# Performance work log

Hardware: AMD Instinct MI355X
Metric: run time of the kernel (lower is better)

The kernel has to match this reference:

```python
import jax, jax.numpy as jnp
import numpy as np

N_NODES = 50000
BN_EPS = 1e-5


def setup_inputs() -> dict:
    key = jax.random.key(0)
    ks = jax.random.split(key, 16)
    N, IN, H, OUT, E = N_NODES, 512, 128, 64, 800000
    s = lambda fi, fo: 1.0 / np.sqrt(fi)
    inp = {
        'x': jax.random.normal(ks[0], (N, IN), dtype=jnp.float32),
        'edge_index': jax.random.randint(ks[1], (2, E), 0, N, dtype=jnp.int32),
        # mlpA: Linear(N -> H)
        'WA': jax.random.uniform(ks[2], (H, N), jnp.float32, -s(N, H), s(N, H)),
        'bA': jax.random.uniform(ks[3], (H,), jnp.float32, -s(N, H), s(N, H)),
        # mlpX: Linear(IN -> H)
        'WX': jax.random.uniform(ks[4], (H, IN), jnp.float32, -s(IN, H), s(IN, H)),
        'bX': jax.random.uniform(ks[5], (H,), jnp.float32, -s(IN, H), s(IN, H)),
        # W: Linear(2H -> H)
        'W': jax.random.uniform(ks[6], (H, 2 * H), jnp.float32, -s(2 * H, H), s(2 * H, H)),
        'bW': jax.random.uniform(ks[7], (H,), jnp.float32, -s(2 * H, H), s(2 * H, H)),
        # mlp_final layer 1: Linear(H -> H) + BN
        'Wf1': jax.random.uniform(ks[8], (H, H), jnp.float32, -s(H, H), s(H, H)),
        'bf1': jax.random.uniform(ks[9], (H,), jnp.float32, -s(H, H), s(H, H)),
        'gamma': jnp.ones((H,), jnp.float32),
        'beta': jnp.zeros((H,), jnp.float32),
        # mlp_final layer 2: Linear(H -> OUT)
        'Wf2': jax.random.uniform(ks[10], (OUT, H), jnp.float32, -s(H, OUT), s(H, OUT)),
        'bf2': jax.random.uniform(ks[11], (OUT,), jnp.float32, -s(H, OUT), s(H, OUT)),
    }
    return inp


def _batchnorm(x, gamma, beta):
    # training-mode BN over the node/batch axis (biased variance, as in torch)
    mean = jnp.mean(x, axis=0)
    var = jnp.var(x, axis=0)
    return (x - mean) * jax.lax.rsqrt(var + BN_EPS) * gamma + beta


def reference(x, edge_index, WA, bA, WX, bX, W, bW, Wf1, bf1, gamma, beta, Wf2, bf2):
    row, col = edge_index[0], edge_index[1]
    row = row - row.min()
    # xA = A @ WA.T + bA  where A[i,j]=1 per (row,col) edge (duplicates sum).
    # Equivalent SpMM: gather columns of WA at `col`, segment-sum into `row`.
    xA = jax.ops.segment_sum(WA.T[col], row, num_segments=N_NODES) + bA  # [N, H]
    xX = x @ WX.T + bX  # [N, H]
    h = jnp.concatenate([xA, xX], axis=-1) @ W.T + bW  # [N, H]
    h = jax.nn.relu(h + xA + xX)
    # mlp_final (num_layers=2): Linear -> ReLU -> BN -> (dropout off) -> Linear
    h = jax.nn.relu(h @ Wf1.T + bf1)
    h = _batchnorm(h, gamma, beta)
    out = h @ Wf2.T + bf2  # [N, OUT]
    return out
```

## Files before the change

kernel.cpp:

```cpp
#include <hip/hip_runtime.h>

typedef __bf16 bf16_t;
typedef __bf16 bf16x8 __attribute__((ext_vector_type(8)));
typedef __bf16 bf16x2 __attribute__((ext_vector_type(2)));
typedef float f32x4 __attribute__((ext_vector_type(4)));

#define IN_DIM 512
#define H_DIM 128
#define OUT_DIM 64
#define BN_EPS 1e-5f
#define SCAN_BLK 2048

#define MFMA(a, b, c) __builtin_amdgcn_mfma_f32_16x16x32_bf16(a, b, c, 0, 0, 0)

__device__ __forceinline__ int detect_bf(const void* gamma) {
    return (*(const unsigned*)gamma == 0x3F803F80u) ? 1 : 0;
}

__device__ __forceinline__ float ld_adapt(const void* p, size_t i, int isbf) {
    return isbf ? (float)((const bf16_t*)p)[i] : ((const float*)p)[i];
}

__device__ __forceinline__ void split8(const float* p, bf16x8& hi, bf16x8& lo) {
    f32x4 v0 = *(const f32x4*)p;
    f32x4 v1 = *(const f32x4*)(p + 4);
#pragma unroll
    for (int i = 0; i < 8; ++i) {
        float f = (i < 4) ? v0[i] : v1[i - 4];
        bf16_t h = (bf16_t)f;
        hi[i] = h;
        lo[i] = (bf16_t)(f - (float)h);
    }
}

__device__ __forceinline__ void split8v(const f32x4& v0, const f32x4& v1, bf16x8& hi, bf16x8& lo) {
#pragma unroll
    for (int i = 0; i < 8; ++i) {
        float f = (i < 4) ? v0[i] : v1[i - 4];
        bf16_t h = (bf16_t)f;
        hi[i] = h;
        lo[i] = (bf16_t)(f - (float)h);
    }
}

__global__ __launch_bounds__(256) void k_transpose(const void* __restrict__ WA,
                                                   void* __restrict__ WAT, int N,
                                                   const void* __restrict__ gamma) {
    __shared__ float t[64][130];
    int isbf = detect_bf(gamma);
    int n0 = blockIdx.x * 64;
    int tid = threadIdx.x;
#pragma unroll
    for (int i = 0; i < 32; ++i) {
        int lin = i * 256 + tid;
        int h = lin >> 6, nl = lin & 63;
        int n = n0 + nl;
        t[nl][h] = (n < N) ? ld_adapt(WA, (size_t)h * N + n, isbf) : 0.f;
    }
    __syncthreads();
#pragma unroll
    for (int i = 0; i < 32; ++i) {
        int lin = i * 256 + tid;
        int nl = lin >> 7, h = lin & 127;
        int n = n0 + nl;
        if (n < N) {
            float v = t[nl][h];
            if (isbf)
                ((bf16_t*)WAT)[(size_t)n * H_DIM + h] = (bf16_t)v;
            else
                ((float*)WAT)[(size_t)n * H_DIM + h] = v;
        }
    }
}

__global__ __launch_bounds__(256) void k_prep(const int* __restrict__ rows, int E,
                                              int* __restrict__ bmin, int* __restrict__ cnt) {
    __shared__ int sm[4];
    int i = blockIdx.x * 256 + threadIdx.x;
    int m = 0x7fffffff;
    if (i < E) {
        int r = rows[i];
        m = r;
        atomicAdd(&cnt[r], 1);
    }
    for (int off = 32; off; off >>= 1) m = min(m, __shfl_xor(m, off, 64));
    if ((threadIdx.x & 63) == 0) sm[threadIdx.x >> 6] = m;
    __syncthreads();
    if (threadIdx.x == 0)
        bmin[blockIdx.x] = min(min(sm[0], sm[1]), min(sm[2], sm[3]));
}

__global__ __launch_bounds__(256) void k_scan1(const int* __restrict__ cnt,
                                               int* __restrict__ offs,
                                               int* __restrict__ bsum, int N) {
    __shared__ int ts[256];
    int base = blockIdx.x * SCAN_BLK;
    int t = threadIdx.x;
    int v[8], s = 0;
#pragma unroll
    for (int i = 0; i < 8; ++i) {
        int idx = base + t * 8 + i;
        v[i] = (idx < N) ? cnt[idx] : 0;
        s += v[i];
    }
    ts[t] = s;
    __syncthreads();
    for (int off = 1; off < 256; off <<= 1) {
        int x = (t >= off) ? ts[t - off] : 0;
        __syncthreads();
        ts[t] += x;
        __syncthreads();
    }
    int run = ts[t] - s;
#pragma unroll
    for (int i = 0; i < 8; ++i) {
        int idx = base + t * 8 + i;
        if (idx < N) offs[idx] = run;
        run += v[i];
    }
    if (t == 255) bsum[blockIdx.x] = ts[255];
}

__global__ __launch_bounds__(256) void k_scan2(int* __restrict__ bsum, int* __restrict__ offs,
                                               int NB, int N, const int* __restrict__ bmin,
                                               int nbmin, int* __restrict__ minbuf) {
    __shared__ int sm[256];
    int t = threadIdx.x;
    int m = 0x7fffffff;
    for (int i = t; i < nbmin; i += 256) m = min(m, bmin[i]);
    sm[t] = m;
    __syncthreads();
    for (int off = 128; off; off >>= 1) {
        if (t < off) sm[t] = min(sm[t], sm[t + off]);
        __syncthreads();
    }
    if (t == 0) {
        *minbuf = sm[0];
        int run = 0;
        for (int b = 0; b < NB; ++b) {
            int v = bsum[b];
            bsum[b] = run;
            run += v;
        }
        offs[N] = run;
    }
}

__global__ __launch_bounds__(256) void k_scan3(int* __restrict__ offs, const int* __restrict__ bsum,
                                               int* __restrict__ cursor, int N) {
    int i = blockIdx.x * 256 + threadIdx.x;
    if (i >= N) return;
    int v = offs[i] + bsum[i / SCAN_BLK];
    offs[i] = v;
    cursor[i] = v;
}

__global__ __launch_bounds__(256) void k_build(const int* __restrict__ rows,
                                               const int* __restrict__ cols, int E,
                                               int* __restrict__ cursor,
                                               int* __restrict__ scol) {
    int i = blockIdx.x * 256 + threadIdx.x;
    if (i >= E) return;
    int r = rows[i];
    int pos = atomicAdd(&cursor[r], 1);
    scol[pos] = cols[i];
}

__global__ __launch_bounds__(256) void k_gather(const int* __restrict__ offs,
                                                const int* __restrict__ scol,
                                                const void* __restrict__ WAT,
                                                const void* __restrict__ bA,
                                                const int* __restrict__ minbuf,
                                                float* __restrict__ xA, int N,
                                                const void* __restrict__ gamma) {
    int isbf = detect_bf(gamma);
    int wave = threadIdx.x >> 6, lane = threadIdx.x & 63;
    int r = blockIdx.x * 4 + wave;
    if (r >= N) return;
    int b = r + *minbuf;
    int s = 0, e = 0;
    if (b < N) {
        s = offs[b];
        e = offs[b + 1];
    }
    float2 a0 = {0.f, 0.f}, a1 = {0.f, 0.f}, a2 = {0.f, 0.f}, a3 = {0.f, 0.f};
    int i = s;
    if (isbf) {
        const bf16_t* Wb = (const bf16_t*)WAT;
        for (; i + 7 < e; i += 8) {
            bf16x2 w[8];
#pragma unroll
            for (int j = 0; j < 8; ++j) {
                int c = scol[i + j];
                w[j] = *(const bf16x2*)(Wb + (size_t)c * H_DIM + lane * 2);
            }
            a0.x += (float)w[0][0] + (float)w[4][0]; a0.y += (float)w[0][1] + (float)w[4][1];
            a1.x += (float)w[1][0] + (float)w[5][0]; a1.y += (float)w[1][1] + (float)w[5][1];
            a2.x += (float)w[2][0] + (float)w[6][0]; a2.y += (float)w[2][1] + (float)w[6][1];
            a3.x += (float)w[3][0] + (float)w[7][0]; a3.y += (float)w[3][1] + (float)w[7][1];
        }
        for (; i < e; ++i) {
            int c = scol[i];
            bf16x2 w = *(const bf16x2*)(Wb + (size_t)c * H_DIM + lane * 2);
            a0.x += (float)w[0]; a0.y += (float)w[1];
        }
    } else {
        const float* Wf = (const float*)WAT;
        for (; i + 7 < e; i += 8) {
            float2 w[8];
#pragma unroll
            for (int j = 0; j < 8; ++j) {
                int c = scol[i + j];
                w[j] = *(const float2*)(Wf + (size_t)c * H_DIM + lane * 2);
            }
            a0.x += w[0].x + w[4].x; a0.y += w[0].y + w[4].y;
            a1.x += w[1].x + w[5].x; a1.y += w[1].y + w[5].y;
            a2.x += w[2].x + w[6].x; a2.y += w[2].y + w[6].y;
            a3.x += w[3].x + w[7].x; a3.y += w[3].y + w[7].y;
        }
        for (; i < e; ++i) {
            int c = scol[i];
            float2 w = *(const float2*)(Wf + (size_t)c * H_DIM + lane * 2);
            a0.x += w.x; a0.y += w.y;
        }
    }
    float bx = ld_adapt(bA, lane * 2, isbf);
    float by = ld_adapt(bA, lane * 2 + 1, isbf);
    float2 out = {a0.x + a1.x + a2.x + a3.x + bx, a0.y + a1.y + a2.y + a3.y + by};
    *(float2*)(xA + (size_t)r * H_DIM + lane * 2) = out;
}

__device__ __forceinline__ void pack_frag(const void* __restrict__ W, bf16_t* __restrict__ hi,
                                          bf16_t* __restrict__ lo, int K, int NC,
                                          int addres, int isbf, int f, int lane) {
    int ks = f / (NC >> 4), nt = f % (NC >> 4);
    int n = nt * 16 + (lane & 15);
    int k0 = ks * 32 + (lane >> 4) * 8;
    bf16_t* dh = hi + (size_t)f * 512 + lane * 8;
    bf16_t* dl = lo + (size_t)f * 512 + lane * 8;
#pragma unroll
    for (int j = 0; j < 8; ++j) {
        int kk = k0 + j;
        float v = ld_adapt(W, (size_t)n * K + kk, isbf);
        if (addres && (kk == n || kk == n + H_DIM)) v += 1.f;
        bf16_t h = (bf16_t)v;
        dh[j] = h;
        dl[j] = (bf16_t)(v - (float)h);
    }
}

__global__ __launch_bounds__(256) void k_pack3(const void* WX, bf16_t* WXh, bf16_t* WXl,
                                               const void* W, bf16_t* Wh, bf16_t* Wl,
                                               const void* Wf1, bf16_t* Wf1h, bf16_t* Wf1l,
                                               const void* __restrict__ gamma) {
    int g = blockIdx.x * 256 + threadIdx.x;
    int f = g >> 6, lane = g & 63;
    int isbf = detect_bf(gamma);
    if (f < 128)
        pack_frag(WX, WXh, WXl, IN_DIM, H_DIM, 0, isbf, f, lane);
    else if (f < 192)
        pack_frag(W, Wh, Wl, 2 * H_DIM, H_DIM, 1, isbf, f - 128, lane);
    else if (f < 224)
        pack_frag(Wf1, Wf1h, Wf1l, H_DIM, H_DIM, 0, isbf, f - 192, lane);
}

template <int ISBF>
__device__ __forceinline__ void fuseA_body(
    const void* __restrict__ x, const float* __restrict__ xAf,
    const bf16_t* __restrict__ WXh, const bf16_t* __restrict__ WXl,
    const bf16_t* __restrict__ Wh, const bf16_t* __restrict__ Wl,
    const bf16_t* __restrict__ Wf1h, const bf16_t* __restrict__ Wf1l,
    const void* __restrict__ bX, const void* __restrict__ bWv, const void* __restrict__ bf1,
    float* __restrict__ h2, double* __restrict__ sums, double* __restrict__ sumsq,
    float* ax, float* ls_sum, float* ls_sq, int M) {
    int tid = threadIdx.x;
    int wave = tid >> 6, lane = tid & 63, l16 = lane & 15, quad = lane >> 4;
    int band = wave & 1, half = wave >> 1;
    int ntb = half * 4;
    int mbase = blockIdx.x * 32 + band * 16;
    int r0 = min(mbase + l16, M - 1);

    if (tid < H_DIM) {
        ls_sum[tid] = 0.f;
        ls_sq[tid] = 0.f;
    }

    f32x4 acc[4];
    bf16x8 pb[2][4];

    auto loadB4 = [&](const bf16_t* __restrict__ H, int fb, bf16x8 dst[4]) {
        const bf16_t* hp = H + (size_t)fb * 512 + lane * 8;
#pragma unroll
        for (int nt = 0; nt < 4; ++nt) dst[nt] = *(const bf16x8*)(hp + nt * 512);
    };

#pragma unroll
    for (int nt = 0; nt < 4; ++nt) acc[nt] = f32x4{0.f, 0.f, 0.f, 0.f};
    if (ISBF) {
        const bf16_t* xb = (const bf16_t*)x + (size_t)r0 * IN_DIM + quad * 8;
        bf16x8 a[16];
#pragma unroll
        for (int ks = 0; ks < 16; ++ks) a[ks] = *(const bf16x8*)(xb + ks * 32);
        loadB4(WXh, ntb, pb[0]);
#pragma unroll
        for (int ks = 0; ks < 16; ++ks) {
            int cur = ks & 1;
            if (ks < 15) loadB4(WXh, (ks + 1) * 8 + ntb, pb[cur ^ 1]);
#pragma unroll
            for (int nt = 0; nt < 4; ++nt) acc[nt] = MFMA(a[ks], pb[cur][nt], acc[nt]);
        }
    } else {
        const float* xf = (const float*)x + (size_t)r0 * IN_DIM + quad * 8;
        bf16x8 bl4[4];
        for (int ks = 0; ks < 16; ++ks) {
            bf16x8 ah, al;
            split8(xf + ks * 32, ah, al);
            loadB4(WXh, ks * 8 + ntb, pb[0]);
            loadB4(WXl, ks * 8 + ntb, bl4);
#pragma unroll
            for (int nt = 0; nt < 4; ++nt) {
                acc[nt] = MFMA(ah, pb[0][nt], acc[nt]);
                acc[nt] = MFMA(ah, bl4[nt], acc[nt]);
                acc[nt] = MFMA(al, pb[0][nt], acc[nt]);
            }
        }
    }
#pragma unroll
    for (int nt = 0; nt < 4; ++nt) {
        int col = (ntb + nt) * 16 + l16;
        float b = ld_adapt(bX, col, ISBF);
#pragma unroll
        for (int r = 0; r < 4; ++r) {
            int lr = band * 16 + quad * 4 + r;
            ax[lr * 132 + col] = acc[nt][r] + b;
        }
    }
    __syncthreads();

#pragma unroll
    for (int nt = 0; nt < 4; ++nt) acc[nt] = f32x4{0.f, 0.f, 0.f, 0.f};
    {
        size_t aoff = (size_t)r0 * H_DIM + quad * 8;
        const float* axp = ax + (band * 16 + l16) * 132 + quad * 8;
        f32x4 pa[8];
#pragma unroll
        for (int i = 0; i < 8; ++i) pa[i] = *(const f32x4*)(xAf + aoff + (i >> 1) * 32 + (i & 1) * 4);
        bf16x8 bl4[4];
        loadB4(Wh, ntb, pb[0]);
#pragma unroll
        for (int ks = 0; ks < 8; ++ks) {
            int cur = ks & 1;
            if (ks < 7) loadB4(Wh, (ks + 1) * 8 + ntb, pb[cur ^ 1]);
            bf16x8 ah, al;
            if (ks < 4)
                split8v(pa[2 * ks], pa[2 * ks + 1], ah, al);
            else
                split8(axp + (ks - 4) * 32, ah, al);
            if (!ISBF) loadB4(Wl, ks * 8 + ntb, bl4);
#pragma unroll
            for (int nt = 0; nt < 4; ++nt) {
                acc[nt] = MFMA(ah, pb[cur][nt], acc[nt]);
                acc[nt] = MFMA(al, pb[cur][nt], acc[nt]);
                if (!ISBF) acc[nt] = MFMA(ah, bl4[nt], acc[nt]);
            }
        }
    }
    __syncthreads();
#pragma unroll
    for (int nt = 0; nt < 4; ++nt) {
        int col = (ntb + nt) * 16 + l16;
        float b = ld_adapt(bWv, col, ISBF);
#pragma unroll
        for (int r = 0; r < 4; ++r) {
            int lr = band * 16 + quad * 4 + r;
            ax[lr * 132 + col] = fmaxf(acc[nt][r] + b, 0.f);
        }
    }
    __syncthreads();

#pragma unroll
    for (int nt = 0; nt < 4; ++nt) acc[nt] = f32x4{0.f, 0.f, 0.f, 0.f};
    {
        const float* axp = ax + (band * 16 + l16) * 132 + quad * 8;
        bf16x8 bl4[4];
        loadB4(Wf1h, ntb, pb[0]);
#pragma unroll
        for (int ks = 0; ks < 4; ++ks) {
            int cur = ks & 1;
            if (ks < 3) loadB4(Wf1h, (ks + 1) * 8 + ntb, pb[cur ^ 1]);
            bf16x8 ah, al;
            split8(axp + ks * 32, ah, al);
            if (!ISBF) loadB4(Wf1l, ks * 8 + ntb, bl4);
#pragma unroll
            for (int nt = 0; nt < 4; ++nt) {
                acc[nt] = MFMA(ah, pb[cur][nt], acc[nt]);
                acc[nt] = MFMA(al, pb[cur][nt], acc[nt]);
                if (!ISBF) acc[nt] = MFMA(ah, bl4[nt], acc[nt]);
            }
        }
    }
#pragma unroll
    for (int nt = 0; nt < 4; ++nt) {
        int col = (ntb + nt) * 16 + l16;
        float b = ld_adapt(bf1, col, ISBF);
        float s = 0.f, s2 = 0.f;
#pragma unroll
        for (int r = 0; r < 4; ++r) {
            int row = mbase + quad * 4 + r;
            if (row < M) {
                float v = fmaxf(acc[nt][r] + b, 0.f);
                h2[(size_t)row * H_DIM + col] = v;
                s += v;
                s2 += v * v;
            }
        }
        s += __shfl_xor(s, 16, 64);
        s += __shfl_xor(s, 32, 64);
        s2 += __shfl_xor(s2, 16, 64);
        s2 += __shfl_xor(s2, 32, 64);
        if (quad == 0) {
            atomicAdd(&ls_sum[col], s);
            atomicAdd(&ls_sq[col], s2);
        }
    }
    __syncthreads();
    if (tid < H_DIM) {
        atomicAdd(&sums[tid], (double)ls_sum[tid]);
        atomicAdd(&sumsq[tid], (double)ls_sq[tid]);
    }
}

__global__ __launch_bounds__(256, 4) void k_fuseA(
    const void* __restrict__ x, const float* __restrict__ xAf,
    const bf16_t* __restrict__ WXh, const bf16_t* __restrict__ WXl,
    const bf16_t* __restrict__ Wh, const bf16_t* __restrict__ Wl,
    const bf16_t* __restrict__ Wf1h, const bf16_t* __restrict__ Wf1l,
    const void* __restrict__ bX, const void* __restrict__ bWv, const void* __restrict__ bf1,
    float* __restrict__ h2, double* __restrict__ sums, double* __restrict__ sumsq,
    const void* __restrict__ gamma, int M) {
    __shared__ float ax[32 * 132];
    __shared__ float ls_sum[H_DIM], ls_sq[H_DIM];
    if (detect_bf(gamma))
        fuseA_body<1>(x, xAf, WXh, WXl, Wh, Wl, Wf1h, Wf1l, bX, bWv, bf1, h2, sums, sumsq,
                      ax, ls_sum, ls_sq, M);
    else
        fuseA_body<0>(x, xAf, WXh, WXl, Wh, Wl, Wf1h, Wf1l, bX, bWv, bf1, h2, sums, sumsq,
                      ax, ls_sum, ls_sq, M);
}

__global__ __launch_bounds__(256) void k_fuseB(
    const float* __restrict__ h2, const void* __restrict__ Wf2,
    const void* __restrict__ gamma, const void* __restrict__ beta, const void* __restrict__ bf2,
    const double* __restrict__ sums, const double* __restrict__ sumsq,
    void* __restrict__ outv, int M) {
    __shared__ bf16_t wh[16 * 512];
    __shared__ bf16_t wl[16 * 512];
    __shared__ float aw[H_DIM], cw[H_DIM], b2[OUT_DIM];
    int t = threadIdx.x;
    int isbf = detect_bf(gamma);

    if (t < H_DIM) {
        double mean = sums[t] / (double)M;
        double var = sumsq[t] / (double)M - mean * mean;
        if (var < 0) var = 0;
        float a = ld_adapt(gamma, t, isbf) * rsqrtf((float)var + BN_EPS);
        aw[t] = a;
        cw[t] = ld_adapt(beta, t, isbf) - (float)mean * a;
    }
    __syncthreads();
    if (t < OUT_DIM) {
        float acc = ld_adapt(bf2, t, isbf);
        for (int j = 0; j < H_DIM; ++j) acc += ld_adapt(Wf2, (size_t)t * H_DIM + j, isbf) * cw[j];
        b2[t] = acc;
    }
    for (int u = t; u < 1024; u += 256) {
        int f = u >> 6, ln = u & 63;
        int ks = f >> 2, nt = f & 3;
        int n = nt * 16 + (ln & 15);
        int k0 = ks * 32 + (ln >> 4) * 8;
#pragma unroll
        for (int j = 0; j < 8; ++j) {
            float v = ld_adapt(Wf2, (size_t)n * H_DIM + k0 + j, isbf) * aw[k0 + j];
            bf16_t h = (bf16_t)v;
            wh[f * 512 + ln * 8 + j] = h;
            wl[f * 512 + ln * 8 + j] = (bf16_t)(v - (float)h);
        }
    }
    __syncthreads();

    int wave = t >> 6, lane = t & 63, l16 = lane & 15, quad = lane >> 4;
    int mbase = blockIdx.x * 64 + wave * 16;
    int r0 = min(mbase + l16, M - 1);
    f32x4 ph[8];
#pragma unroll
    for (int i = 0; i < 8; ++i)
        ph[i] = *(const f32x4*)(h2 + (size_t)r0 * H_DIM + quad * 8 + (i >> 1) * 32 + (i & 1) * 4);
    f32x4 acc4[4];
#pragma unroll
    for (int nt = 0; nt < 4; ++nt) acc4[nt] = f32x4{0.f, 0.f, 0.f, 0.f};
#pragma unroll
    for (int ks = 0; ks < 4; ++ks) {
        bf16x8 ah, al;
        split8v(ph[2 * ks], ph[2 * ks + 1], ah, al);
#pragma unroll
        for (int nt = 0; nt < 4; ++nt) {
            bf16x8 bh = *(const bf16x8*)(wh + (ks * 4 + nt) * 512 + lane * 8);
            bf16x8 bl = *(const bf16x8*)(wl + (ks * 4 + nt) * 512 + lane * 8);
            acc4[nt] = MFMA(ah, bh, acc4[nt]);
            acc4[nt] = MFMA(ah, bl, acc4[nt]);
            acc4[nt] = MFMA(al, bh, acc4[nt]);
        }
    }
#pragma unroll
    for (int nt = 0; nt < 4; ++nt) {
        int col = nt * 16 + l16;
        float b = b2[col];
#pragma unroll
        for (int r = 0; r < 4; ++r) {
            int row = mbase + quad * 4 + r;
            if (row < M) {
                float v = acc4[nt][r] + b;
                if (isbf)
                    ((bf16_t*)outv)[(size_t)row * OUT_DIM + col] = (bf16_t)v;
                else
                    ((float*)outv)[(size_t)row * OUT_DIM + col] = v;
            }
        }
    }
}

extern "C" void kernel_launch(void* const* d_in, const int* in_sizes, int n_in,
                              void* d_out, int out_size, void* d_ws, size_t ws_size,
                              hipStream_t stream) {
    const void* x = d_in[0];
    const int* ei = (const int*)d_in[1];
    const void* WA = d_in[2];
    const void* bA = d_in[3];
    const void* WX = d_in[4];
    const void* bX = d_in[5];
    const void* W = d_in[6];
    const void* bW = d_in[7];
    const void* Wf1 = d_in[8];
    const void* bf1 = d_in[9];
    const void* gamma = d_in[10];
    const void* beta = d_in[11];
    const void* Wf2 = d_in[12];
    const void* bf2 = d_in[13];

    const int N = in_sizes[0] / IN_DIM;
    const int E = in_sizes[1] / 2;
    const int* rows = ei;
    const int* cols = ei + E;
    const int eblocks = (E + 255) / 256;

    char* ws = (char*)d_ws;
    size_t off = 0;
    auto alloc = [&](size_t bytes) {
        char* p = ws + off;
        off += (bytes + 255) & ~(size_t)255;
        return p;
    };
    int* minbuf = (int*)alloc(4);
    double* sums = (double*)alloc(2 * H_DIM * 8);
    double* sumsq = sums + H_DIM;
    bf16_t* WXp_h = (bf16_t*)alloc((size_t)IN_DIM * H_DIM * 2);
    bf16_t* WXp_l = (bf16_t*)alloc((size_t)IN_DIM * H_DIM * 2);
    bf16_t* Wp_h = (bf16_t*)alloc((size_t)256 * H_DIM * 2);
    bf16_t* Wp_l = (bf16_t*)alloc((size_t)256 * H_DIM * 2);
    bf16_t* Wf1p_h = (bf16_t*)alloc((size_t)H_DIM * H_DIM * 2);
    bf16_t* Wf1p_l = (bf16_t*)alloc((size_t)H_DIM * H_DIM * 2);
    int* cnt = (int*)alloc((size_t)N * 4);
    int* offs = (int*)alloc(((size_t)N + 1) * 4);
    int* cursor = (int*)alloc((size_t)N * 4);
    int* bsum = (int*)alloc(64 * 4);
    int* bmin = (int*)alloc((size_t)eblocks * 4);
    int* scol = (int*)alloc((size_t)E * 4);
    void* WAT = (void*)alloc((size_t)N * H_DIM * 4);
    float* xAf = (float*)alloc((size_t)N * H_DIM * 4);
    float* h2 = (float*)WAT;

    hipMemsetAsync(cnt, 0, (size_t)N * 4, stream);
    hipMemsetAsync(sums, 0, 2 * H_DIM * 8, stream);

    k_transpose<<<(N + 63) / 64, 256, 0, stream>>>(WA, WAT, N, gamma);
    k_pack3<<<56, 256, 0, stream>>>(WX, WXp_h, WXp_l, W, Wp_h, Wp_l, Wf1, Wf1p_h, Wf1p_l, gamma);

    k_prep<<<eblocks, 256, 0, stream>>>(rows, E, bmin, cnt);
    int NB = (N + SCAN_BLK - 1) / SCAN_BLK;
    k_scan1<<<NB, 256, 0, stream>>>(cnt, offs, bsum, N);
    k_scan2<<<1, 256, 0, stream>>>(bsum, offs, NB, N, bmin, eblocks, minbuf);
    k_scan3<<<(N + 255) / 256, 256, 0, stream>>>(offs, bsum, cursor, N);
    k_build<<<eblocks, 256, 0, stream>>>(rows, cols, E, cursor, scol);
    k_gather<<<(N + 3) / 4, 256, 0, stream>>>(offs, scol, WAT, bA, minbuf, xAf, N, gamma);

    k_fuseA<<<(N + 31) / 32, 256, 0, stream>>>(x, xAf, WXp_h, WXp_l, Wp_h, Wp_l, Wf1p_h, Wf1p_l,
                                               bX, bW, bf1, h2, sums, sumsq, gamma, N);
    k_fuseB<<<(N + 63) / 64, 256, 0, stream>>>(h2, Wf2, gamma, beta, bf2, sums, sumsq, d_out, N);
}
```

Baseline: 497.2 us.

## Fuse SpMM gather into fuseA and merge transpose with weight packing

The standalone gather kernel is folded into k_fuseA. Each block now computes its 32 rows of xA straight into shared memory, so the xA intermediate is never written to or read back from global memory. The transpose and pack kernels are merged into a single launch. fuseA now streams its x fragments with double buffering instead of preloading all sixteen, fuseB reads h2 directly instead of preloading it into registers, and fuseA's launch bound no longer requests four blocks per CU. The cost is more shared memory per block and a serial, low-parallelism gather phase inside the MFMA kernel, which may lower occupancy and latency hiding.

Result: no change. 495.3 us (-0.4%).

```diff
diff --git a/kernel.cpp b/kernel.cpp
--- a/kernel.cpp
+++ b/kernel.cpp
@@ -33,23 +33,46 @@
     }
 }
 
-__device__ __forceinline__ void split8v(const f32x4& v0, const f32x4& v1, bf16x8& hi, bf16x8& lo) {
-#pragma unroll
-    for (int i = 0; i < 8; ++i) {
-        float f = (i < 4) ? v0[i] : v1[i - 4];
-        bf16_t h = (bf16_t)f;
-        hi[i] = h;
-        lo[i] = (bf16_t)(f - (float)h);
-    }
-}
-
-__global__ __launch_bounds__(256) void k_transpose(const void* __restrict__ WA,
-                                                   void* __restrict__ WAT, int N,
-                                                   const void* __restrict__ gamma) {
+__device__ __forceinline__ void pack_frag(const void* __restrict__ W, bf16_t* __restrict__ hi,
+                                          bf16_t* __restrict__ lo, int K, int NC,
+                                          int addres, int isbf, int f, int lane) {
+    int ks = f / (NC >> 4), nt = f % (NC >> 4);
+    int n = nt * 16 + (lane & 15);
+    int k0 = ks * 32 + (lane >> 4) * 8;
+    bf16_t* dh = hi + (size_t)f * 512 + lane * 8;
+    bf16_t* dl = lo + (size_t)f * 512 + lane * 8;
+#pragma unroll
+    for (int j = 0; j < 8; ++j) {
+        int kk = k0 + j;
+        float v = ld_adapt(W, (size_t)n * K + kk, isbf);
+        if (addres && (kk == n || kk == n + H_DIM)) v += 1.f;
+        bf16_t h = (bf16_t)v;
+        dh[j] = h;
+        dl[j] = (bf16_t)(v - (float)h);
+    }
+}
+
+__global__ __launch_bounds__(256) void k_transpack(
+    const void* __restrict__ WA, void* __restrict__ WAT, int N, int TB,
+    const void* WX, bf16_t* WXh, bf16_t* WXl,
+    const void* W, bf16_t* Wh, bf16_t* Wl,
+    const void* Wf1, bf16_t* Wf1h, bf16_t* Wf1l,
+    const void* __restrict__ gamma) {
     __shared__ float t[64][130];
     int isbf = detect_bf(gamma);
+    int tid = threadIdx.x;
+    if (blockIdx.x >= TB) {
+        int g = (blockIdx.x - TB) * 256 + tid;
+        int f = g >> 6, lane = g & 63;
+        if (f < 128)
+            pack_frag(WX, WXh, WXl, IN_DIM, H_DIM, 0, isbf, f, lane);
+        else if (f < 192)
+            pack_frag(W, Wh, Wl, 2 * H_DIM, H_DIM, 1, isbf, f - 128, lane);
+        else if (f < 224)
+            pack_frag(Wf1, Wf1h, Wf1l, H_DIM, H_DIM, 0, isbf, f - 192, lane);
+        return;
+    }
     int n0 = blockIdx.x * 64;
-    int tid = threadIdx.x;
 #pragma unroll
     for (int i = 0; i < 32; ++i) {
         int lin = i * 256 + tid;
@@ -166,113 +189,16 @@
     scol[pos] = cols[i];
 }
 
-__global__ __launch_bounds__(256) void k_gather(const int* __restrict__ offs,
-                                                const int* __restrict__ scol,
-                                                const void* __restrict__ WAT,
-                                                const void* __restrict__ bA,
-                                                const int* __restrict__ minbuf,
-                                                float* __restrict__ xA, int N,
-                                                const void* __restrict__ gamma) {
-    int isbf = detect_bf(gamma);
-    int wave = threadIdx.x >> 6, lane = threadIdx.x & 63;
-    int r = blockIdx.x * 4 + wave;
-    if (r >= N) return;
-    int b = r + *minbuf;
-    int s = 0, e = 0;
-    if (b < N) {
-        s = offs[b];
-        e = offs[b + 1];
-    }
-    float2 a0 = {0.f, 0.f}, a1 = {0.f, 0.f}, a2 = {0.f, 0.f}, a3 = {0.f, 0.f};
-    int i = s;
-    if (isbf) {
-        const bf16_t* Wb = (const bf16_t*)WAT;
-        for (; i + 7 < e; i += 8) {
-            bf16x2 w[8];
-#pragma unroll
-            for (int j = 0; j < 8; ++j) {
-                int c = scol[i + j];
-                w[j] = *(const bf16x2*)(Wb + (size_t)c * H_DIM + lane * 2);
-            }
-            a0.x += (float)w[0][0] + (float)w[4][0]; a0.y += (float)w[0][1] + (float)w[4][1];
-            a1.x += (float)w[1][0] + (float)w[5][0]; a1.y += (float)w[1][1] + (float)w[5][1];
-            a2.x += (float)w[2][0] + (float)w[6][0]; a2.y += (float)w[2][1] + (float)w[6][1];
-            a3.x += (float)w[3][0] + (float)w[7][0]; a3.y += (float)w[3][1] + (float)w[7][1];
-        }
-        for (; i < e; ++i) {
-            int c = scol[i];
-            bf16x2 w = *(const bf16x2*)(Wb + (size_t)c * H_DIM + lane * 2);
-            a0.x += (float)w[0]; a0.y += (float)w[1];
-        }
-    } else {
-        const float* Wf = (const float*)WAT;
-        for (; i + 7 < e; i += 8) {
-            float2 w[8];
-#pragma unroll
-            for (int j = 0; j < 8; ++j) {
-                int c = scol[i + j];
-                w[j] = *(const float2*)(Wf + (size_t)c * H_DIM + lane * 2);
-            }
-            a0.x += w[0].x + w[4].x; a0.y += w[0].y + w[4].y;
-            a1.x += w[1].x + w[5].x; a1.y += w[1].y + w[5].y;
-            a2.x += w[2].x + w[6].x; a2.y += w[2].y + w[6].y;
-            a3.x += w[3].x + w[7].x; a3.y += w[3].y + w[7].y;
-        }
-        for (; i < e; ++i) {
-            int c = scol[i];
-            float2 w = *(const float2*)(Wf + (size_t)c * H_DIM + lane * 2);
-            a0.x += w.x; a0.y += w.y;
-        }
-    }
-    float bx = ld_adapt(bA, lane * 2, isbf);
-    float by = ld_adapt(bA, lane * 2 + 1, isbf);
-    float2 out = {a0.x + a1.x + a2.x + a3.x + bx, a0.y + a1.y + a2.y + a3.y + by};
-    *(float2*)(xA + (size_t)r * H_DIM + lane * 2) = out;
-}
-
-__device__ __forceinline__ void pack_frag(const void* __restrict__ W, bf16_t* __restrict__ hi,
-                                          bf16_t* __restrict__ lo, int K, int NC,
-                                          int addres, int isbf, int f, int lane) {
-    int ks = f / (NC >> 4), nt = f % (NC >> 4);
-    int n = nt * 16 + (lane & 15);
-    int k0 = ks * 32 + (lane >> 4) * 8;
-    bf16_t* dh = hi + (size_t)f * 512 + lane * 8;
-    bf16_t* dl = lo + (size_t)f * 512 + lane * 8;
-#pragma unroll
-    for (int j = 0; j < 8; ++j) {
-        int kk = k0 + j;
-        float v = ld_adapt(W, (size_t)n * K + kk, isbf);
-        if (addres && (kk == n || kk == n + H_DIM)) v += 1.f;
-        bf16_t h = (bf16_t)v;
-        dh[j] = h;
-        dl[j] = (bf16_t)(v - (float)h);
-    }
-}
-
-__global__ __launch_bounds__(256) void k_pack3(const void* WX, bf16_t* WXh, bf16_t* WXl,
-                                               const void* W, bf16_t* Wh, bf16_t* Wl,
-                                               const void* Wf1, bf16_t* Wf1h, bf16_t* Wf1l,
-                                               const void* __restrict__ gamma) {
-    int g = blockIdx.x * 256 + threadIdx.x;
-    int f = g >> 6, lane = g & 63;
-    int isbf = detect_bf(gamma);
-    if (f < 128)
-        pack_frag(WX, WXh, WXl, IN_DIM, H_DIM, 0, isbf, f, lane);
-    else if (f < 192)
-        pack_frag(W, Wh, Wl, 2 * H_DIM, H_DIM, 1, isbf, f - 128, lane);
-    else if (f < 224)
-        pack_frag(Wf1, Wf1h, Wf1l, H_DIM, H_DIM, 0, isbf, f - 192, lane);
-}
-
 template <int ISBF>
 __device__ __forceinline__ void fuseA_body(
-    const void* __restrict__ x, const float* __restrict__ xAf,
+    const void* __restrict__ x, const int* __restrict__ offs, const int* __restrict__ scol,
+    const void* __restrict__ WAT, const void* __restrict__ bA, const int* __restrict__ minbuf,
     const bf16_t* __restrict__ WXh, const bf16_t* __restrict__ WXl,
     const bf16_t* __restrict__ Wh, const bf16_t* __restrict__ Wl,
     const bf16_t* __restrict__ Wf1h, const bf16_t* __restrict__ Wf1l,
     const void* __restrict__ bX, const void* __restrict__ bWv, const void* __restrict__ bf1,
     float* __restrict__ h2, double* __restrict__ sums, double* __restrict__ sumsq,
-    float* ax, float* ls_sum, float* ls_sq, int M) {
+    float* axA, float* axx, float* ls_sum, float* ls_sq, int M, int N) {
     int tid = threadIdx.x;
     int wave = tid >> 6, lane = tid & 63, l16 = lane & 15, quad = lane >> 4;
     int band = wave & 1, half = wave >> 1;
@@ -285,9 +211,69 @@
         ls_sq[tid] = 0.f;
     }
 
+    {
+        int rmin = *minbuf;
+        float bx = ld_adapt(bA, lane * 2, ISBF);
+        float by = ld_adapt(bA, lane * 2 + 1, ISBF);
+        for (int i = 0; i < 8; ++i) {
+            int lr = wave * 8 + i;
+            int rg = blockIdx.x * 32 + lr;
+            float ax_ = 0.f, ay_ = 0.f, bx2 = 0.f, by2 = 0.f;
+            if (rg < M) {
+                int b = rg + rmin;
+                int s = 0, en = 0;
+                if (b < N) {
+                    s = offs[b];
+                    en = offs[b + 1];
+                }
+                int e = s;
+                if (ISBF) {
+                    const bf16_t* Wb = (const bf16_t*)WAT;
+                    for (; e + 3 < en; e += 4) {
+                        int c0 = scol[e], c1 = scol[e + 1], c2 = scol[e + 2], c3 = scol[e + 3];
+                        bf16x2 w0 = *(const bf16x2*)(Wb + (size_t)c0 * H_DIM + lane * 2);
+                        bf16x2 w1 = *(const bf16x2*)(Wb + (size_t)c1 * H_DIM + lane * 2);
+                        bf16x2 w2 = *(const bf16x2*)(Wb + (size_t)c2 * H_DIM + lane * 2);
+                        bf16x2 w3 = *(const bf16x2*)(Wb + (size_t)c3 * H_DIM + lane * 2);
+                        ax_ += (float)w0[0] + (float)w2[0];
+                        ay_ += (float)w0[1] + (float)w2[1];
+                        bx2 += (float)w1[0] + (float)w3[0];
+                        by2 += (float)w1[1] + (float)w3[1];
+                    }
+                    for (; e < en; ++e) {
+                        int c = scol[e];
+                        bf16x2 w = *(const bf16x2*)(Wb + (size_t)c * H_DIM + lane * 2);
+                        ax_ += (float)w[0];
+                        ay_ += (float)w[1];
+                    }
+                } else {
+                    const float* Wf = (const float*)WAT;
+                    for (; e + 3 < en; e += 4) {
+                        int c0 = scol[e], c1 = scol[e + 1], c2 = scol[e + 2], c3 = scol[e + 3];
+                        float2 w0 = *(const float2*)(Wf + (size_t)c0 * H_DIM + lane * 2);
+                        float2 w1 = *(const float2*)(Wf + (size_t)c1 * H_DIM + lane * 2);
+                        float2 w2 = *(const float2*)(Wf + (size_t)c2 * H_DIM + lane * 2);
+                        float2 w3 = *(const float2*)(Wf + (size_t)c3 * H_DIM + lane * 2);
+                        ax_ += w0.x + w2.x;
+                        ay_ += w0.y + w2.y;
+                        bx2 += w1.x + w3.x;
+                        by2 += w1.y + w3.y;
+                    }
+                    for (; e < en; ++e) {
+                        int c = scol[e];
+                        float2 w = *(const float2*)(Wf + (size_t)c * H_DIM + lane * 2);
+                        ax_ += w.x;
+                        ay_ += w.y;
+                    }
+                }
+            }
+            axA[lr * 132 + lane * 2] = ax_ + bx2 + bx;
+            axA[lr * 132 + lane * 2 + 1] = ay_ + by2 + by;
+        }
+    }
+
     f32x4 acc[4];
     bf16x8 pb[2][4];
-
     auto loadB4 = [&](const bf16_t* __restrict__ H, int fb, bf16x8 dst[4]) {
         const bf16_t* hp = H + (size_t)fb * 512 + lane * 8;
 #pragma unroll
@@ -298,16 +284,18 @@
     for (int nt = 0; nt < 4; ++nt) acc[nt] = f32x4{0.f, 0.f, 0.f, 0.f};
     if (ISBF) {
         const bf16_t* xb = (const bf16_t*)x + (size_t)r0 * IN_DIM + quad * 8;
-        bf16x8 a[16];
-#pragma unroll
-        for (int ks = 0; ks < 16; ++ks) a[ks] = *(const bf16x8*)(xb + ks * 32);
+        bf16x8 a[2];
+        a[0] = *(const bf16x8*)xb;
         loadB4(WXh, ntb, pb[0]);
 #pragma unroll
         for (int ks = 0; ks < 16; ++ks) {
             int cur = ks & 1;
-            if (ks < 15) loadB4(WXh, (ks + 1) * 8 + ntb, pb[cur ^ 1]);
-#pragma unroll
-            for (int nt = 0; nt < 4; ++nt) acc[nt] = MFMA(a[ks], pb[cur][nt], acc[nt]);
+            if (ks < 15) {
+                a[cur ^ 1] = *(const bf16x8*)(xb + (ks + 1) * 32);
+                loadB4(WXh, (ks + 1) * 8 + ntb, pb[cur ^ 1]);
+            }
+#pragma unroll
+            for (int nt = 0; nt < 4; ++nt) acc[nt] = MFMA(a[cur], pb[cur][nt], acc[nt]);
         }
     } else {
         const float* xf = (const float*)x + (size_t)r0 * IN_DIM + quad * 8;
@@ -332,7 +320,7 @@
 #pragma unroll
         for (int r = 0; r < 4; ++r) {
             int lr = band * 16 + quad * 4 + r;
-            ax[lr * 132 + col] = acc[nt][r] + b;
+            axx[lr * 132 + col] = acc[nt][r] + b;
         }
     }
     __syncthreads();
@@ -340,11 +328,8 @@
 #pragma unroll
     for (int nt = 0; nt < 4; ++nt) acc[nt] = f32x4{0.f, 0.f, 0.f, 0.f};
     {
-        size_t aoff = (size_t)r0 * H_DIM + quad * 8;
-        const float* axp = ax + (band * 16 + l16) * 132 + quad * 8;
-        f32x4 pa[8];
-#pragma unroll
-        for (int i = 0; i < 8; ++i) pa[i] = *(const f32x4*)(xAf + aoff + (i >> 1) * 32 + (i & 1) * 4);
+        const float* apA = axA + (band * 16 + l16) * 132 + quad * 8;
+        const float* apX = axx + (band * 16 + l16) * 132 + quad * 8;
         bf16x8 bl4[4];
         loadB4(Wh, ntb, pb[0]);
 #pragma unroll
@@ -353,9 +338,9 @@
             if (ks < 7) loadB4(Wh, (ks + 1) * 8 + ntb, pb[cur ^ 1]);
             bf16x8 ah, al;
             if (ks < 4)
-                split8v(pa[2 * ks], pa[2 * ks + 1], ah, al);
+                split8(apA + ks * 32, ah, al);
             else
-                split8(axp + (ks - 4) * 32, ah, al);
+                split8(apX + (ks - 4) * 32, ah, al);
             if (!ISBF) loadB4(Wl, ks * 8 + ntb, bl4);
 #pragma unroll
             for (int nt = 0; nt < 4; ++nt) {
@@ -373,7 +358,7 @@
 #pragma unroll
         for (int r = 0; r < 4; ++r) {
             int lr = band * 16 + quad * 4 + r;
-            ax[lr * 132 + col] = fmaxf(acc[nt][r] + b, 0.f);
+            axx[lr * 132 + col] = fmaxf(acc[nt][r] + b, 0.f);
         }
     }
     __syncthreads();
@@ -381,7 +366,7 @@
 #pragma unroll
     for (int nt = 0; nt < 4; ++nt) acc[nt] = f32x4{0.f, 0.f, 0.f, 0.f};
     {
-        const float* axp = ax + (band * 16 + l16) * 132 + quad * 8;
+        const float* axp = axx + (band * 16 + l16) * 132 + quad * 8;
         bf16x8 bl4[4];
         loadB4(Wf1h, ntb, pb[0]);
 #pragma unroll
@@ -430,22 +415,24 @@
     }
 }
 
-__global__ __launch_bounds__(256, 4) void k_fuseA(
-    const void* __restrict__ x, const float* __restrict__ xAf,
+__global__ __launch_bounds__(256) void k_fuseA(
+    const void* __restrict__ x, const int* __restrict__ offs, const int* __restrict__ scol,
+    const void* __restrict__ WAT, const void* __restrict__ bA, const int* __restrict__ minbuf,
     const bf16_t* __restrict__ WXh, const bf16_t* __restrict__ WXl,
     const bf16_t* __restrict__ Wh, const bf16_t* __restrict__ Wl,
     const bf16_t* __restrict__ Wf1h, const bf16_t* __restrict__ Wf1l,
     const void* __restrict__ bX, const void* __restrict__ bWv, const void* __restrict__ bf1,
     float* __restrict__ h2, double* __restrict__ sums, double* __restrict__ sumsq,
-    const void* __restrict__ gamma, int M) {
-    __shared__ float ax[32 * 132];
+    const void* __restrict__ gamma, int M, int N) {
+    __shared__ float axA[32 * 132];
+    __shared__ float axx[32 * 132];
     __shared__ float ls_sum[H_DIM], ls_sq[H_DIM];
     if (detect_bf(gamma))
-        fuseA_body<1>(x, xAf, WXh, WXl, Wh, Wl, Wf1h, Wf1l, bX, bWv, bf1, h2, sums, sumsq,
-                      ax, ls_sum, ls_sq, M);
+        fuseA_body<1>(x, offs, scol, WAT, bA, minbuf, WXh, WXl, Wh, Wl, Wf1h, Wf1l, bX, bWv, bf1,
+                      h2, sums, sumsq, axA, axx, ls_sum, ls_sq, M, N);
     else
-        fuseA_body<0>(x, xAf, WXh, WXl, Wh, Wl, Wf1h, Wf1l, bX, bWv, bf1, h2, sums, sumsq,
-                      ax, ls_sum, ls_sq, M);
+        fuseA_body<0>(x, offs, scol, WAT, bA, minbuf, WXh, WXl, Wh, Wl, Wf1h, Wf1l, bX, bWv, bf1,
+                      h2, sums, sumsq, axA, axx, ls_sum, ls_sq, M, N);
 }
 
 __global__ __launch_bounds__(256) void k_fuseB(
@@ -491,17 +478,13 @@
     int wave = t >> 6, lane = t & 63, l16 = lane & 15, quad = lane >> 4;
     int mbase = blockIdx.x * 64 + wave * 16;
     int r0 = min(mbase + l16, M - 1);
-    f32x4 ph[8];
-#pragma unroll
-    for (int i = 0; i < 8; ++i)
-        ph[i] = *(const f32x4*)(h2 + (size_t)r0 * H_DIM + quad * 8 + (i >> 1) * 32 + (i & 1) * 4);
     f32x4 acc4[4];
 #pragma unroll
     for (int nt = 0; nt < 4; ++nt) acc4[nt] = f32x4{0.f, 0.f, 0.f, 0.f};
 #pragma unroll
     for (int ks = 0; ks < 4; ++ks) {
         bf16x8 ah, al;
-        split8v(ph[2 * ks], ph[2 * ks + 1], ah, al);
+        split8(h2 + (size_t)r0 * H_DIM + ks * 32 + quad * 8, ah, al);
 #pragma unroll
         for (int nt = 0; nt < 4; ++nt) {
             bf16x8 bh = *(const bf16x8*)(wh + (ks * 4 + nt) * 512 + lane * 8);
@@ -576,14 +559,14 @@
     int* bmin = (int*)alloc((size_t)eblocks * 4);
     int* scol = (int*)alloc((size_t)E * 4);
     void* WAT = (void*)alloc((size_t)N * H_DIM * 4);
-    float* xAf = (float*)alloc((size_t)N * H_DIM * 4);
-    float* h2 = (float*)WAT;
+    float* h2 = (float*)alloc((size_t)N * H_DIM * 4);
 
     hipMemsetAsync(cnt, 0, (size_t)N * 4, stream);
     hipMemsetAsync(sums, 0, 2 * H_DIM * 8, stream);
 
-    k_transpose<<<(N + 63) / 64, 256, 0, stream>>>(WA, WAT, N, gamma);
-    k_pack3<<<56, 256, 0, stream>>>(WX, WXp_h, WXp_l, W, Wp_h, Wp_l, Wf1, Wf1p_h, Wf1p_l, gamma);
+    int TB = (N + 63) / 64;
+    k_transpack<<<TB + 56, 256, 0, stream>>>(WA, WAT, N, TB, WX, WXp_h, WXp_l, W, Wp_h, Wp_l,
+                                             Wf1, Wf1p_h, Wf1p_l, gamma);
 
     k_prep<<<eblocks, 256, 0, stream>>>(rows, E, bmin, cnt);
     int NB = (N + SCAN_BLK - 1) / SCAN_BLK;
@@ -591,9 +574,9 @@
     k_scan2<<<1, 256, 0, stream>>>(bsum, offs, NB, N, bmin, eblocks, minbuf);
     k_scan3<<<(N + 255) / 256, 256, 0, stream>>>(offs, bsum, cursor, N);
     k_build<<<eblocks, 256, 0, stream>>>(rows, cols, E, cursor, scol);
-    k_gather<<<(N + 3) / 4, 256, 0, stream>>>(offs, scol, WAT, bA, minbuf, xAf, N, gamma);
-
-    k_fuseA<<<(N + 31) / 32, 256, 0, stream>>>(x, xAf, WXp_h, WXp_l, Wp_h, Wp_l, Wf1p_h, Wf1p_l,
-                                               bX, bW, bf1, h2, sums, sumsq, gamma, N);
+
+    k_fuseA<<<(N + 31) / 32, 256, 0, stream>>>(x, offs, scol, WAT, bA, minbuf,
+                                               WXp_h, WXp_l, Wp_h, Wp_l, Wf1p_h, Wf1p_l,
+                                               bX, bW, bf1, h2, sums, sumsq, gamma, N, N);
     k_fuseB<<<(N + 63) / 64, 256, 0, stream>>>(h2, Wf2, gamma, beta, bf2, sums, sumsq, d_out, N);
 }
```
